# Kernel tuning notes

Hardware: AMD Instinct MI355X
Metric: run time of the kernel (lower is better)

Reference implementation:

```python
import jax, jax.numpy as jnp
import numpy as np

NEG_INF = float(-2 ** 31)
B, S, D_IN, D_H, H = 4, 2048, 512, 512, 8


def setup_inputs() -> dict:
    key = jax.random.key(0)
    ks = jax.random.split(key, 11)
    sc_in = 1.0 / np.sqrt(D_IN)
    sc_pr = 1.0 / np.sqrt(D_H * H)
    x = jax.random.normal(ks[0], (B, S, D_IN), dtype=jnp.float32)
    mask = jax.random.randint(ks[1], (B, 1, S), 0, 2, dtype=jnp.int32)
    Wq = jax.random.uniform(ks[2], (H, D_IN, D_H), jnp.float32, -sc_in, sc_in)
    bq = jax.random.uniform(ks[3], (H, D_H), jnp.float32, -sc_in, sc_in)
    Wk = jax.random.uniform(ks[4], (H, D_IN, D_H), jnp.float32, -sc_in, sc_in)
    bk = jax.random.uniform(ks[5], (H, D_H), jnp.float32, -sc_in, sc_in)
    Wv = jax.random.uniform(ks[6], (H, D_IN, D_H), jnp.float32, -sc_in, sc_in)
    bv = jax.random.uniform(ks[7], (H, D_H), jnp.float32, -sc_in, sc_in)
    Wp = jax.random.uniform(ks[8], (H * D_H, D_H), jnp.float32, -sc_pr, sc_pr)
    bp = jax.random.uniform(ks[9], (D_H,), jnp.float32, -sc_pr, sc_pr)
    return {"x": x, "mask": mask, "Wq": Wq, "bq": bq, "Wk": Wk, "bk": bk,
            "Wv": Wv, "bv": bv, "Wp": Wp, "bp": bp}


def reference(x, mask, Wq, bq, Wk, bk, Wv, bv, Wp, bp):
    # per-head Q/K/V projections, batched over the head axis h
    q = jnp.einsum('bsd,hde->bhse', x, Wq) + bq[None, :, None, :]
    k = jnp.einsum('bsd,hde->bhse', x, Wk) + bk[None, :, None, :]
    v = jnp.einsum('bsd,hde->bhse', x, Wv) + bv[None, :, None, :]
    scores = jnp.einsum('bhse,bhte->bhst', q, k) / jnp.sqrt(jnp.float32(D_H))
    scores = jnp.where(mask[:, None, :, :] == 0, NEG_INF, scores)
    probs = jax.nn.softmax(scores, axis=-1)
    out = jnp.einsum('bhst,bhte->bhse', probs, v)  # [B,H,S,D_H]
    cat = out.transpose(0, 2, 1, 3).reshape(B, S, H * D_H)
    return cat @ Wp + bp
```

## Files before the change

### kernel.cpp

```cpp
#include <hip/hip_runtime.h>
#include <hip/hip_bf16.h>
#include <cstdint>
#include <cstddef>

typedef unsigned short ushort_t;
typedef __bf16 bf16x8 __attribute__((ext_vector_type(8)));
typedef float floatx4 __attribute__((ext_vector_type(4)));

#define S_LEN 2048
#define DIN   512
#define DH    512
#define NHEAD 8
#define NBAT  4
#define NBH   32
#define HP    4096

#define MiB (1024ull * 1024ull)
#define WQT_OFF   (0ull)
#define WKT_OFF   (4ull  * MiB)
#define WVT_OFF   (8ull  * MiB)
#define WPT_OFF   (12ull * MiB)
#define XBF_OFF   (16ull * MiB)
#define Q_OFF     (24ull * MiB)
#define K_OFF     (88ull * MiB)
#define VT_OFF    (152ull * MiB)
#define O_OFF     (216ull * MiB)
#define LSUM_OFF  (280ull * MiB)
#define P_OFF     (281ull * MiB)
#define WS_BYTES  (409ull * MiB)

__device__ __align__(256) unsigned char g_ws[WS_BYTES];

__device__ __forceinline__ ushort_t f2bf(float f) {
  union { float f; uint32_t u; } v; v.f = f;
  uint32_t r = v.u + 0x7fffu + ((v.u >> 16) & 1u);
  return (ushort_t)(r >> 16);
}

typedef __attribute__((address_space(3))) uint32_t lds_uint;
typedef __attribute__((address_space(1))) const uint32_t glb_uint;

__device__ __forceinline__ void async16(void* lds, const void* g) {
  __builtin_amdgcn_global_load_lds((glb_uint*)g, (lds_uint*)lds, 16, 0, 0);
}

#define BBAR() do { \
    __builtin_amdgcn_sched_barrier(0); \
    __builtin_amdgcn_s_barrier(); \
    __builtin_amdgcn_sched_barrier(0); \
  } while (0)


#define STG_A(dbuf, hh, kt) do { \
    const ushort_t* _g = gA + (size_t)(kt) * 64 + (size_t)(hh) * a128; \
    char* _s = sAh + (dbuf) * 32768 + (hh) * 16384; \
    async16(_s, _g); \
    async16(_s + 8192, _g + a64); \
  } while (0)

#define STG_B(dbuf, hh, kt) do { \
    const ushort_t* _g = gB + (size_t)(kt) * 64 + (size_t)(hh) * b128; \
    char* _s = sBh + (dbuf) * 32768 + (hh) * 16384; \
    async16(_s, _g); \
    async16(_s + 8192, _g + b64); \
  } while (0)

#define LD_A2(dst, buf, qm) do { \
    const char* _b = (const char*)As + (buf) * 32768 + (qm) * 16384 + aoff0; \
    _Pragma("unroll") \
    for (int _i = 0; _i < 4; ++_i) { \
      dst[_i][0] = *(const bf16x8*)(_b + (_i << 11) + swz0); \
      dst[_i][1] = *(const bf16x8*)(_b + (_i << 11) + swz1); \
    } } while (0)

#define LD_B2(dst, buf, qn) do { \
    const char* _b = (const char*)Bs + (buf) * 32768 + (qn) * 16384 + boff0; \
    _Pragma("unroll") \
    for (int _j = 0; _j < 2; ++_j) { \
      dst[_j][0] = *(const bf16x8*)(_b + (_j << 11) + swz0); \
      dst[_j][1] = *(const bf16x8*)(_b + (_j << 11) + swz1); \
    } } while (0)

#define MM(q, AF, BF) do { \
    _Pragma("unroll") \
    for (int _i = 0; _i < 4; ++_i) { \
      _Pragma("unroll") \
      for (int _j = 0; _j < 2; ++_j) { \
        acc[q][_i][_j] = __builtin_amdgcn_mfma_f32_16x16x32_bf16(AF[_i][0], BF[_j][0], acc[q][_i][_j], 0, 0, 0); \
        acc[q][_i][_j] = __builtin_amdgcn_mfma_f32_16x16x32_bf16(AF[_i][1], BF[_j][1], acc[q][_i][_j], 0, 0, 0); \
      } \
    } \
  } while (0)

__device__ __forceinline__ void gemm256_core(
    const ushort_t* __restrict__ A, const ushort_t* __restrict__ Bt,
    int lda, int ldb, int kdim,
    ushort_t* As, ushort_t* Bs, floatx4 acc[4][4][2])
{
  const int t = threadIdx.x;
  const int w = t >> 6, l = t & 63;
  const int l15 = l & 15, lq = l >> 4;
  const int wq_r = w >> 2, wq_c = w & 3;

  const int r0 = t >> 3, c0 = t & 7;
  const ushort_t* gA = A + (size_t)r0 * lda + ((c0 ^ (r0 & 7)) << 3);
  const ushort_t* gB = Bt + (size_t)r0 * ldb + ((c0 ^ (r0 & 7)) << 3);
  const size_t a64 = (size_t)64 * lda, b64 = (size_t)64 * ldb;
  const size_t a128 = (size_t)128 * lda, b128 = (size_t)128 * ldb;
  char* sAh = (char*)As + (w << 10);
  char* sBh = (char*)Bs + (w << 10);

  const int aoff0 = ((wq_r << 6) + l15) << 7;
  const int boff0 = ((wq_c << 5) + l15) << 7;
  const int l7 = l15 & 7;
  const int swz0 = (lq ^ l7) << 4;
  const int swz1 = ((4 + lq) ^ l7) << 4;

  const int nt = kdim >> 6;

#pragma unroll
  for (int q = 0; q < 4; ++q)
#pragma unroll
    for (int i = 0; i < 4; ++i)
#pragma unroll
      for (int j = 0; j < 2; ++j)
        acc[q][i][j] = (floatx4){0.f, 0.f, 0.f, 0.f};

  STG_A(0, 0, 0);
  STG_A(0, 1, 0);
  STG_B(0, 0, 0);
  STG_B(0, 1, 0);
  asm volatile("s_waitcnt vmcnt(0)" ::: "memory");
  BBAR();

  bf16x8 a0[4][2], a1[4][2], b0[2][2], b1[2][2];

  LD_B2(b0, 0, 0);
  LD_A2(a0, 0, 0);

#pragma unroll 1
  for (int tt = 0; tt < nt; ++tt) {
    const int cur = tt & 1, nxt = cur ^ 1;
    __builtin_amdgcn_s_setprio(1);
    LD_B2(b1, cur, 1);
    if (tt + 1 < nt) {
      STG_A(nxt, 0, tt + 1);
      STG_A(nxt, 1, tt + 1);
      STG_B(nxt, 0, tt + 1);
      STG_B(nxt, 1, tt + 1);
    }
    MM(0, a0, b0);
    LD_A2(a1, cur, 1);
    MM(1, a0, b1);
    MM(2, a1, b1);
    MM(3, a1, b0);
    __builtin_amdgcn_s_setprio(0);
    asm volatile("s_waitcnt vmcnt(0)" ::: "memory");
    BBAR();
    if (tt + 1 < nt) {
      LD_B2(b0, nxt, 0);
      LD_A2(a0, nxt, 0);
    }
  }
}

__device__ __forceinline__ void gemm_core(
    const ushort_t* __restrict__ A, const ushort_t* __restrict__ Bt,
    int lda, int ldb, int kdim,
    ushort_t* As, ushort_t* Bs, floatx4 acc[4][4])
{
  const int t = threadIdx.x;
  const int w = t >> 6;
  const int l = t & 63;
  const int wrow = w >> 1, wcol = w & 1;
  const int l15 = l & 15, lq = l >> 4;

  const ushort_t* gA = A + (size_t)(t >> 2) * lda + (t & 3) * 8;
  const ushort_t* gB = Bt + (size_t)(t >> 2) * ldb + (t & 3) * 8;
  const size_t strideA = (size_t)64 * lda;
  const size_t strideB = (size_t)64 * ldb;
  char* ldsA0 = (char*)As + w * 1024;
  char* ldsB0 = (char*)Bs + w * 1024;

  async16(ldsA0,        gA);
  async16(ldsA0 + 4096, gA + strideA);
  async16(ldsB0,        gB);
  async16(ldsB0 + 4096, gB + strideB);

#pragma unroll
  for (int i = 0; i < 4; ++i)
#pragma unroll
    for (int j = 0; j < 4; ++j)
      acc[i][j] = (floatx4){0.f, 0.f, 0.f, 0.f};

  const int nwin = kdim >> 5;
#pragma unroll 1
  for (int k = 0; k < nwin; ++k) {
    __syncthreads();
    const int cur = k & 1;
    if (k + 1 < nwin) {
      const int nxt = cur ^ 1;
      const ushort_t* gA1 = gA + (size_t)(k + 1) * 32;
      const ushort_t* gB1 = gB + (size_t)(k + 1) * 32;
      char* ldsA1 = ldsA0 + nxt * 8192;
      char* ldsB1 = ldsB0 + nxt * 8192;
      async16(ldsA1,        gA1);
      async16(ldsA1 + 4096, gA1 + strideA);
      async16(ldsB1,        gB1);
      async16(ldsB1 + 4096, gB1 + strideB);
    }
    const ushort_t* rdA = As + cur * 4096 + (wrow * 64 + l15) * 32 + lq * 8;
    const ushort_t* rdB = Bs + cur * 4096 + (wcol * 64 + l15) * 32 + lq * 8;

    bf16x8 af[4], bfr[4];
#pragma unroll
    for (int i = 0; i < 4; ++i) af[i] = *(const bf16x8*)(rdA + i * 512);
#pragma unroll
    for (int j = 0; j < 4; ++j) bfr[j] = *(const bf16x8*)(rdB + j * 512);
#pragma unroll
    for (int i = 0; i < 4; ++i)
#pragma unroll
      for (int j = 0; j < 4; ++j)
        acc[i][j] = __builtin_amdgcn_mfma_f32_16x16x32_bf16(af[i], bfr[j], acc[i][j], 0, 0, 0);
  }
}

__global__ __launch_bounds__(256) void convert_f32_bf16(
    const float* __restrict__ src, size_t dstOff, int n)
{
  ushort_t* dst = (ushort_t*)(g_ws + dstOff);
  int i = (blockIdx.x * 256 + threadIdx.x) * 4;
  if (i >= n) return;
  float4 v = *(const float4*)(src + i);
  ushort_t o[4] = {f2bf(v.x), f2bf(v.y), f2bf(v.z), f2bf(v.w)};
  *(uint2*)(dst + i) = *(const uint2*)o;
}

__global__ __launch_bounds__(256) void transpose_f32_bf16(
    const float* __restrict__ src, size_t dstOff, int R, int C)
{
  __shared__ ushort_t tile[32][33];
  ushort_t* dst = (ushort_t*)(g_ws + dstOff) + (size_t)blockIdx.z * R * C;
  src += (size_t)blockIdx.z * R * C;
  int r0 = blockIdx.y * 32, c0 = blockIdx.x * 32;
  int tx = threadIdx.x & 31, ty = threadIdx.x >> 5;
  for (int i = ty; i < 32; i += 8)
    tile[i][tx] = f2bf(src[(size_t)(r0 + i) * C + (c0 + tx)]);
  __syncthreads();
  for (int i = ty; i < 32; i += 8)
    dst[(size_t)(c0 + i) * R + (r0 + tx)] = tile[tx][i];
}

__global__ __launch_bounds__(256) void zero_lsum()
{
  float* lsum = (float*)(g_ws + LSUM_OFF);
  int i = (blockIdx.x * 256 + threadIdx.x) * 4;
  *(float4*)(lsum + i) = (float4){0.f, 0.f, 0.f, 0.f};
}

__global__ __launch_bounds__(512, 2) void qkv_gemm(
    const float* __restrict__ bq, const float* __restrict__ bk,
    const float* __restrict__ bv)
{
  __shared__ __align__(16) ushort_t SH[65536];
  ushort_t* As = SH;
  ushort_t* Bs = SH + 32768;
  const int z = blockIdx.z;
  const int bh = z & 31, sel = z >> 5, b = bh >> 3, h = bh & 7;
  const size_t wOff = (sel == 0) ? WQT_OFF : (sel == 1) ? WKT_OFF : WVT_OFF;
  const float* bias = ((sel == 0) ? bq : (sel == 1) ? bk : bv) + h * DH;
  const int tileM = blockIdx.y * 256, tileN = blockIdx.x * 256;

  const ushort_t* A  = (const ushort_t*)(g_ws + XBF_OFF)
                       + ((size_t)b * S_LEN + tileM) * DIN;
  const ushort_t* Bt = (const ushort_t*)(g_ws + wOff)
                       + ((size_t)h * DH + tileN) * DIN;
  floatx4 acc[4][4][2];
  gemm256_core(A, Bt, DIN, DIN, DIN, As, Bs, acc);

  const int t = threadIdx.x, w = t >> 6, l = t & 63;
  const int l15 = l & 15, lq = l >> 4;
  const int wq_r = w >> 2, wq_c = w & 3;
  const int QM[4] = {0, 0, 1, 1}, QN[4] = {0, 1, 1, 0};

  if (sel == 2) {
    char* SB = (char*)SH;
#pragma unroll
    for (int q = 0; q < 4; ++q) {
#pragma unroll
      for (int j = 0; j < 2; ++j) {
        const int nl = QN[q] * 128 + wq_c * 32 + j * 16 + l15;
        const float bsn = bias[tileN + nl];
#pragma unroll
        for (int i = 0; i < 4; ++i) {
          const int ml = QM[q] * 128 + wq_r * 64 + i * 16 + lq * 4;
          ushort_t pk[4];
#pragma unroll
          for (int r = 0; r < 4; ++r) pk[r] = f2bf(acc[q][i][j][r] + bsn);
          const int byte = nl * 512 + (((ml >> 3) ^ (nl & 7)) << 4) + (ml & 7) * 2;
          *(uint2*)(SB + byte) = *(const uint2*)pk;
        }
      }
    }
    BBAR();
    ushort_t* VTb = (ushort_t*)(g_ws + VT_OFF)
                    + ((size_t)bh * DH + tileN) * S_LEN + tileM;
#pragma unroll
    for (int s = 0; s < 16; ++s) {
      const int nl = (w << 5) + (s << 1) + (l >> 5);
      const int c  = l & 31;
      const uint4 v = *(const uint4*)(SB + nl * 512 + ((c ^ (nl & 7)) << 4));
      *(uint4*)(VTb + (size_t)nl * S_LEN + c * 8) = v;
    }
  } else {
    ushort_t* Db = (ushort_t*)(g_ws + ((sel == 0) ? Q_OFF : K_OFF));
#pragma unroll
    for (int q = 0; q < 4; ++q) {
#pragma unroll
      for (int j = 0; j < 2; ++j) {
        const int n = tileN + QN[q] * 128 + wq_c * 32 + j * 16 + l15;
        const float bsn = bias[n];
#pragma unroll
        for (int i = 0; i < 4; ++i) {
#pragma unroll
          for (int r = 0; r < 4; ++r) {
            const int m = tileM + QM[q] * 128 + wq_r * 64 + i * 16 + lq * 4 + r;
            Db[((size_t)bh * S_LEN + m) * DH + n] = f2bf(acc[q][i][j][r] + bsn);
          }
        }
      }
    }
  }
}

__global__ __launch_bounds__(512, 2) void scores_kernel(
    const int* __restrict__ mask, int c0)
{
  __shared__ __align__(16) ushort_t SH[65536];
  ushort_t* As = SH;
  ushort_t* Bs = SH + 32768;
  const int hl = blockIdx.z, bh = c0 + hl, b = bh >> 3;
  const int tileM = blockIdx.y * 256, tileN = blockIdx.x * 256;

  const ushort_t* A  = (const ushort_t*)(g_ws + Q_OFF)
                       + ((size_t)bh * S_LEN + tileM) * DH;
  const ushort_t* Bt = (const ushort_t*)(g_ws + K_OFF)
                       + ((size_t)bh * S_LEN + tileN) * DH;
  floatx4 acc[4][4][2];
  gemm256_core(A, Bt, DH, DH, DH, As, Bs, acc);

  const float scale = 0.04419417382415922f;
  const int t = threadIdx.x, w = t >> 6, l = t & 63;
  const int l15 = l & 15, lq = l >> 4;
  const int wq_r = w >> 2, wq_c = w & 3;
  const int QM[4] = {0, 0, 1, 1}, QN[4] = {0, 1, 1, 0};
  ushort_t* Pp = (ushort_t*)(g_ws + P_OFF) + (size_t)hl * S_LEN * S_LEN;
  const int* mask_b = mask + (size_t)b * S_LEN;
  float* lsum = (float*)(g_ws + LSUM_OFF);

  float rsum[2][4][4];
#pragma unroll
  for (int qm = 0; qm < 2; ++qm)
#pragma unroll
    for (int i = 0; i < 4; ++i)
#pragma unroll
      for (int r = 0; r < 4; ++r) rsum[qm][i][r] = 0.f;

#pragma unroll
  for (int q = 0; q < 4; ++q) {
#pragma unroll
    for (int j = 0; j < 2; ++j) {
      const int n = tileN + QN[q] * 128 + wq_c * 32 + j * 16 + l15;
      const int mv = mask_b[n];
#pragma unroll
      for (int i = 0; i < 4; ++i) {
#pragma unroll
        for (int r = 0; r < 4; ++r) {
          const int m = tileM + QM[q] * 128 + wq_r * 64 + i * 16 + lq * 4 + r;
          float s = fminf(acc[q][i][j][r] * scale, 30.f);
          const float p = mv ? __expf(s) : 0.f;
          rsum[QM[q]][i][r] += p;
          Pp[(size_t)m * S_LEN + n] = f2bf(p);
        }
      }
    }
  }
#pragma unroll
  for (int qm = 0; qm < 2; ++qm) {
#pragma unroll
    for (int i = 0; i < 4; ++i) {
#pragma unroll
      for (int r = 0; r < 4; ++r) {
        float v = rsum[qm][i][r];
        v += __shfl_xor(v, 1);
        v += __shfl_xor(v, 2);
        v += __shfl_xor(v, 4);
        v += __shfl_xor(v, 8);
        if (l15 == 0) {
          const int m = tileM + qm * 128 + wq_r * 64 + i * 16 + lq * 4 + r;
          atomicAdd(&lsum[(size_t)hl * S_LEN + m], v);
        }
      }
    }
  }
}

__global__ __launch_bounds__(512, 2) void pv_kernel(int c0)
{
  __shared__ __align__(16) ushort_t SH[65536];
  ushort_t* As = SH;
  ushort_t* Bs = SH + 32768;
  const int hl = blockIdx.z, bh = c0 + hl, b = bh >> 3, h = bh & 7;
  const int tileM = blockIdx.y * 256, tileN = blockIdx.x * 256;

  const ushort_t* A  = (const ushort_t*)(g_ws + P_OFF)
                       + (size_t)hl * S_LEN * S_LEN + (size_t)tileM * S_LEN;
  const ushort_t* Bt = (const ushort_t*)(g_ws + VT_OFF)
                       + ((size_t)bh * DH + tileN) * S_LEN;
  floatx4 acc[4][4][2];
  gemm256_core(A, Bt, S_LEN, S_LEN, S_LEN, As, Bs, acc);

  const float* lsum = (const float*)(g_ws + LSUM_OFF);
  ushort_t* Ob = (ushort_t*)(g_ws + O_OFF);
  const int t = threadIdx.x, w = t >> 6, l = t & 63;
  const int l15 = l & 15, lq = l >> 4;
  const int wq_r = w >> 2, wq_c = w & 3;
  const int QM[4] = {0, 0, 1, 1}, QN[4] = {0, 1, 1, 0};
#pragma unroll
  for (int q = 0; q < 4; ++q) {
#pragma unroll
    for (int i = 0; i < 4; ++i) {
#pragma unroll
      for (int r = 0; r < 4; ++r) {
        const int m = tileM + QM[q] * 128 + wq_r * 64 + i * 16 + lq * 4 + r;
        const float lv = lsum[(size_t)hl * S_LEN + m];
        const float inv = (lv > 1e-20f) ? 1.0f / lv : 0.f;
#pragma unroll
        for (int j = 0; j < 2; ++j) {
          const int n = tileN + QN[q] * 128 + wq_c * 32 + j * 16 + l15;
          Ob[((size_t)b * S_LEN + m) * HP + h * DH + n] =
              f2bf(acc[q][i][j][r] * inv);
        }
      }
    }
  }
}

__global__ __launch_bounds__(256) void proj_kernel(
    const float* __restrict__ bp, float* __restrict__ out)
{
  __shared__ __align__(16) ushort_t As[2 * 128 * 32], Bs[2 * 128 * 32];
  const int tileM = blockIdx.y * 128, tileN = blockIdx.x * 128;

  const ushort_t* A  = (const ushort_t*)(g_ws + O_OFF) + (size_t)tileM * HP;
  const ushort_t* Bt = (const ushort_t*)(g_ws + WPT_OFF) + (size_t)tileN * HP;
  floatx4 acc[4][4];
  gemm_core(A, Bt, HP, HP, HP, As, Bs, acc);

  const int t = threadIdx.x, w = t >> 6, l = t & 63;
  const int wrow = w >> 1, wcol = w & 1, l15 = l & 15, lq = l >> 4;
#pragma unroll
  for (int j = 0; j < 4; ++j) {
    const int n = tileN + wcol * 64 + j * 16 + l15;
    const float bsn = bp[n];
#pragma unroll
    for (int i = 0; i < 4; ++i) {
#pragma unroll
      for (int r = 0; r < 4; ++r) {
        const int m = tileM + wrow * 64 + i * 16 + lq * 4 + r;
        out[(size_t)m * DH + n] = acc[i][j][r] + bsn;
      }
    }
  }
}

extern "C" void kernel_launch(void* const* d_in, const int* in_sizes, int n_in,
                              void* d_out, int out_size, void* d_ws, size_t ws_size,
                              hipStream_t stream) {
  const float* x  = (const float*)d_in[0];
  const int*   msk= (const int*)d_in[1];
  const float* Wq = (const float*)d_in[2];
  const float* bq = (const float*)d_in[3];
  const float* Wk = (const float*)d_in[4];
  const float* bk = (const float*)d_in[5];
  const float* Wv = (const float*)d_in[6];
  const float* bv = (const float*)d_in[7];
  const float* Wp = (const float*)d_in[8];
  const float* bp = (const float*)d_in[9];
  float* out = (float*)d_out;

  convert_f32_bf16<<<dim3(NBAT * S_LEN * DIN / 1024), 256, 0, stream>>>(
      x, XBF_OFF, NBAT * S_LEN * DIN);

  transpose_f32_bf16<<<dim3(16, 16, NHEAD), 256, 0, stream>>>(Wq, WQT_OFF, DIN, DH);
  transpose_f32_bf16<<<dim3(16, 16, NHEAD), 256, 0, stream>>>(Wk, WKT_OFF, DIN, DH);
  transpose_f32_bf16<<<dim3(16, 16, NHEAD), 256, 0, stream>>>(Wv, WVT_OFF, DIN, DH);
  transpose_f32_bf16<<<dim3(16, 128, 1),    256, 0, stream>>>(Wp, WPT_OFF, HP, DH);

  qkv_gemm<<<dim3(2, 8, 3 * NBH), 512, 0, stream>>>(bq, bk, bv);

  for (int c0 = 0; c0 < NBH; c0 += 16) {
    zero_lsum<<<dim3(32), 256, 0, stream>>>();
    scores_kernel<<<dim3(8, 8, 16), 512, 0, stream>>>(msk, c0);
    pv_kernel<<<dim3(2, 8, 16), 512, 0, stream>>>(c0);
  }

  proj_kernel<<<dim3(DH / 128, (NBAT * S_LEN) / 128), 256, 0, stream>>>(bp, out);
}
```

Measured before the change: 735.0 us.

## Restructure 256x256 GEMM main loop into 8-phase staggered prefetch pipeline

Rewrites the QKV projection GEMM core so that global-to-LDS async loads for the next k-tiles are split into half-tile chunks and issued across four MFMA phases per tile. The loop is unrolled by two tiles and uses partial vmcnt waits instead of draining all loads each iteration. A single A register fragment replaces the previous two. The aim is to overlap memory staging with compute and cut full-drain stalls, at the cost of many more workgroup barriers per tile and trickier buffer-reuse ordering. An extra barrier is added before the V epilogue writes to shared memory.

```diff
diff --git a/kernel.cpp b/kernel.cpp
--- a/kernel.cpp
+++ b/kernel.cpp
@@ -50,6 +50,8 @@
     __builtin_amdgcn_sched_barrier(0); \
   } while (0)
 
+#define RBAR() __builtin_amdgcn_s_barrier()
+
 
 #define STG_A(dbuf, hh, kt) do { \
     const ushort_t* _g = gA + (size_t)(kt) * 64 + (size_t)(hh) * a128; \
@@ -92,6 +94,15 @@
     } \
   } while (0)
 
+#define PHASE(q, AF, BF, STMT) do { \
+    STMT; \
+    RBAR(); \
+    __builtin_amdgcn_s_setprio(1); \
+    MM(q, AF, BF); \
+    __builtin_amdgcn_s_setprio(0); \
+    RBAR(); \
+  } while (0)
+
 __device__ __forceinline__ void gemm256_core(
     const ushort_t* __restrict__ A, const ushort_t* __restrict__ Bt,
     int lda, int ldb, int kdim,
@@ -127,39 +138,52 @@
         acc[q][i][j] = (floatx4){0.f, 0.f, 0.f, 0.f};
 
   STG_A(0, 0, 0);
-  STG_A(0, 1, 0);
   STG_B(0, 0, 0);
   STG_B(0, 1, 0);
-  asm volatile("s_waitcnt vmcnt(0)" ::: "memory");
-  BBAR();
-
-  bf16x8 a0[4][2], a1[4][2], b0[2][2], b1[2][2];
-
-  LD_B2(b0, 0, 0);
-  LD_A2(a0, 0, 0);
+  STG_A(0, 1, 0);
+  STG_A(1, 0, 1);
+  STG_B(1, 0, 1);
+  asm volatile("s_waitcnt vmcnt(4)" ::: "memory");
+  RBAR();
+
+  bf16x8 a[4][2], b0[2][2], b1[2][2];
 
 #pragma unroll 1
-  for (int tt = 0; tt < nt; ++tt) {
-    const int cur = tt & 1, nxt = cur ^ 1;
-    __builtin_amdgcn_s_setprio(1);
-    LD_B2(b1, cur, 1);
-    if (tt + 1 < nt) {
-      STG_A(nxt, 0, tt + 1);
-      STG_A(nxt, 1, tt + 1);
-      STG_B(nxt, 0, tt + 1);
-      STG_B(nxt, 1, tt + 1);
-    }
-    MM(0, a0, b0);
-    LD_A2(a1, cur, 1);
-    MM(1, a0, b1);
-    MM(2, a1, b1);
-    MM(3, a1, b0);
-    __builtin_amdgcn_s_setprio(0);
-    asm volatile("s_waitcnt vmcnt(0)" ::: "memory");
-    BBAR();
-    if (tt + 1 < nt) {
-      LD_B2(b0, nxt, 0);
-      LD_A2(a0, nxt, 0);
+  for (int T = 0; T < nt; T += 2) {
+    const bool more = (T + 2 < nt);
+    LD_A2(a, 0, 0);
+    LD_B2(b0, 0, 0);
+    PHASE(0, a, b0, STG_B(1, 1, T + 1));
+    LD_B2(b1, 0, 1);
+    PHASE(1, a, b1, STG_A(1, 1, T + 1));
+    LD_A2(a, 0, 1);
+    PHASE(2, a, b1, if (more) STG_A(0, 0, T + 2));
+    {
+      if (more) STG_B(0, 0, T + 2);
+      RBAR();
+      __builtin_amdgcn_s_setprio(1);
+      MM(3, a, b0);
+      __builtin_amdgcn_s_setprio(0);
+      if (more) asm volatile("s_waitcnt vmcnt(4)" ::: "memory");
+      else      asm volatile("s_waitcnt vmcnt(0)" ::: "memory");
+      RBAR();
+    }
+    LD_A2(a, 1, 0);
+    LD_B2(b0, 1, 0);
+    PHASE(0, a, b0, if (more) STG_B(0, 1, T + 2));
+    LD_B2(b1, 1, 1);
+    PHASE(1, a, b1, if (more) STG_A(0, 1, T + 2));
+    LD_A2(a, 1, 1);
+    PHASE(2, a, b1, if (more) STG_A(1, 0, T + 3));
+    {
+      if (more) STG_B(1, 0, T + 3);
+      RBAR();
+      __builtin_amdgcn_s_setprio(1);
+      MM(3, a, b0);
+      __builtin_amdgcn_s_setprio(0);
+      if (more) asm volatile("s_waitcnt vmcnt(4)" ::: "memory");
+      else      asm volatile("s_waitcnt vmcnt(0)" ::: "memory");
+      RBAR();
     }
   }
 }
@@ -285,6 +309,7 @@
 
   if (sel == 2) {
     char* SB = (char*)SH;
+    BBAR();
 #pragma unroll
     for (int q = 0; q < 4; ++q) {
 #pragma unroll
```

New measurement: 686.3 us. 6.6% less time.
